# Performance work log

Hardware: AMD Instinct MI355X
Metric: run time of the kernel (lower is better)

Reference implementation:

```python
import jax, jax.numpy as jnp
import numpy as np

# Config constants (mirroring repo globals C.*)
B, L, D = 128, 200, 256          # batch, history length, d_model
NT = 10000                        # num_types (items)
NU = 50000                        # C.USER_NUMBER
NL = 4                            # n_layers
BETA_1 = 0.1                      # C.BETA_1


def _l2norm(x, eps):
    n = jnp.linalg.norm(x, axis=-1, keepdims=True)
    return x / jnp.maximum(n, eps)


def setup_inputs() -> dict:
    key = jax.random.key(0)
    ks = jax.random.split(key, 7)
    user_id = jax.random.randint(ks[0], (B,), 1, NU)
    event_type = jax.random.randint(ks[1], (B, L), 1, NT + 1)  # 1..NT (non-pad)
    adjacent_matrix = jax.random.uniform(ks[2], (NT, NT), jnp.float32)
    pop_encoding = jax.random.normal(ks[3], (NT + 1, D), jnp.float32) * 0.02
    event_emb_w = (jax.random.normal(ks[4], (NT + 1, D), jnp.float32) * 0.02).at[0].set(0.0)
    user_emb_w = (jax.random.normal(ks[5], (NU, D), jnp.float32) * 0.02).at[0].set(0.0)
    layer_ws = jax.random.normal(ks[6], (NL, D, D), jnp.float32) * 0.05
    return {"user_id": user_id, "event_type": event_type,
            "adjacent_matrix": adjacent_matrix, "pop_encoding": pop_encoding,
            "event_emb_w": event_emb_w, "user_emb_w": user_emb_w,
            "layer_ws": layer_ws}


def reference(user_id, event_type, adjacent_matrix, pop_encoding,
              event_emb_w, user_emb_w, layer_ws):
    # non-pad mask (pad idx = 0)
    non_pad = (event_type != 0).astype(jnp.float32)[..., None]  # (B,L,1)

    enc = event_emb_w[event_type]                 # (B,L,D)
    user = user_emb_w[user_id]                    # (B,D)
    pop = pop_encoding[event_type] * non_pad      # (B,L,D)

    # user-specific disentanglement: enc += sign(enc) * normalize(user)
    enc = enc + jnp.sign(enc) * _l2norm(user, 1e-12)[:, None, :]

    # batched adjacency gather: adj[b] = A[e-1][:, e-1] + A[e-1, e-1] (row-broadcast)
    idx = event_type - 1                          # (B,L)
    adj = adjacent_matrix[idx[:, :, None], idx[:, None, :]]      # (B,L,L)
    adj = adj + adjacent_matrix[idx, idx][:, None, :]            # diag broadcast over rows

    # hGCN layer stack: x <- leaky_relu((adj @ x) @ W)
    for i in range(NL):
        enc = jax.nn.leaky_relu(jnp.einsum('bls,bsd->bld', adj, enc) @ layer_ws[i])

    output = enc.mean(axis=1)                     # (B,D)
    user_embeddings = jnp.concatenate([output, pop.mean(axis=1) * BETA_1], axis=-1)  # (B,2D)

    # Predictor (evaluation=True path)
    item_encoding = event_emb_w[1:]               # (NT,D)
    out = user_embeddings[:, :D] @ item_encoding.T  # (B,NT)
    out = _l2norm(out, 1e-5)
    prediction = jnp.tanh(out)
    return prediction, user_embeddings, pop
```

## Files before the change

kernel.cpp:

```cpp
#include <hip/hip_runtime.h>
#include <math.h>

#define B_ 128
#define L_ 200
#define D_ 256
#define NT_ 10000
#define NL_ 4
#define BETA1 0.1f

typedef _Float16 f16x8 __attribute__((ext_vector_type(8)));
typedef _Float16 f16x4 __attribute__((ext_vector_type(4)));
typedef float f32x4 __attribute__((ext_vector_type(4)));

struct HL { _Float16 h, l; };
__device__ __forceinline__ HL split2v(float v) {
    HL r;
    r.h = (_Float16)v;
    r.l = (_Float16)(v - (float)r.h);
    return r;
}

__device__ __forceinline__ float getscale(const unsigned int* amax, int i, int extra) {
    float am = fmaxf(__uint_as_float(amax[i]), 1e-30f);
    return scalbnf(1.f, 6 - ilogbf(am) - extra);
}

__global__ void user_norm_kernel(const int* __restrict__ user_id,
                                 const float* __restrict__ user_emb_w,
                                 float* __restrict__ unorm,
                                 unsigned int* __restrict__ amax) {
    int b = blockIdx.x;
    int d = threadIdx.x;
    if (b == 0 && d < 16) amax[d] = 0u;
    int uid = user_id[b];
    float v = user_emb_w[(long)uid * D_ + d];
    float sq = v * v;
    for (int off = 32; off > 0; off >>= 1) sq += __shfl_down(sq, off, 64);
    __shared__ float s[4];
    int wid = d >> 6, lane = d & 63;
    if (lane == 0) s[wid] = sq;
    __syncthreads();
    float n = sqrtf(s[0] + s[1] + s[2] + s[3]);
    n = fmaxf(n, 1e-12f);
    unorm[b * D_ + d] = v / n;
}

__global__ void enc0pop_kernel(const int* __restrict__ event_type,
                               const float* __restrict__ E,
                               const float* __restrict__ pope,
                               const float* __restrict__ unorm,
                               float* __restrict__ encF,
                               float* __restrict__ pop_out,
                               unsigned int* __restrict__ amax) {
    int d = threadIdx.x;
    float m = 0.f;
    for (int bl = blockIdx.x; bl < B_ * L_; bl += gridDim.x) {
        int b = bl / L_;
        int et = event_type[bl];
        float e = E[(long)et * D_ + d];
        float sg = (e > 0.f) ? 1.f : ((e < 0.f) ? -1.f : 0.f);
        float u = unorm[b * D_ + d];
        float v = e + sg * u;
        encF[(long)bl * D_ + d] = v;
        m = fmaxf(m, fabsf(v));
        pop_out[(long)bl * D_ + d] = (et != 0) ? pope[(long)et * D_ + d] : 0.f;
    }
    for (int off = 32; off > 0; off >>= 1) m = fmaxf(m, __shfl_down(m, off, 64));
    __shared__ float sm[4];
    int wid = d >> 6, lane = d & 63;
    if (lane == 0) sm[wid] = m;
    __syncthreads();
    if (d == 0)
        atomicMax(amax, __float_as_uint(fmaxf(fmaxf(sm[0], sm[1]), fmaxf(sm[2], sm[3]))));
}

__global__ void diag_kernel(const int* __restrict__ event_type,
                            const float* __restrict__ A,
                            float* __restrict__ diag) {
    int i = blockIdx.x * blockDim.x + threadIdx.x;
    if (i >= B_ * L_) return;
    long idx = (long)event_type[i] - 1;
    diag[i] = A[idx * NT_ + idx];
}

__global__ void adj_split_kernel(const int* __restrict__ event_type,
                                 const float* __restrict__ A,
                                 const float* __restrict__ diag,
                                 _Float16* __restrict__ adjH,
                                 _Float16* __restrict__ adjL) {
    int b = blockIdx.y;
    int i0 = blockIdx.x * 4;
    int j = threadIdx.x;
    __shared__ int sidx[L_];
    __shared__ float sdiag[L_];
    if (j < L_) {
        sidx[j]  = event_type[b * L_ + j] - 1;
        sdiag[j] = diag[b * L_ + j];
    }
    __syncthreads();
    if (j >= L_) return;
    float dj = sdiag[j];
    int cj = sidx[j];
#pragma unroll
    for (int r = 0; r < 4; r++) {
        int i = i0 + r;
        float v = A[(long)sidx[i] * NT_ + cj] + dj;
        HL s = split2v(v);
        long o = ((long)b * L_ + i) * L_ + j;
        adjH[o] = s.h; adjL[o] = s.l;
    }
}

__global__ void wsplit_kernel(const float* __restrict__ W,
                              _Float16* __restrict__ WTh,
                              _Float16* __restrict__ WTl) {
    int layer = blockIdx.z;
    int k0 = blockIdx.y * 64, n0 = blockIdx.x * 64;
    const float* Wl = W + (long)layer * D_ * D_;
    __shared__ float t[64][65];
    int tid = threadIdx.x;
    for (int i = 0; i < 16; i++) {
        int idx = i * 256 + tid;
        int k = idx >> 6, n = idx & 63;
        t[k][n] = Wl[(long)(k0 + k) * D_ + n0 + n];
    }
    __syncthreads();
    for (int i = 0; i < 16; i++) {
        int idx = i * 256 + tid;
        int n = idx >> 6, k = idx & 63;
        float v = t[k][n];
        long o = (long)layer * D_ * D_ + (long)(n0 + n) * D_ + (k0 + k);
        HL r = split2v(v);
        WTh[o] = r.h; WTl[o] = r.l;
    }
}

__global__ void esplit_kernel(const float* __restrict__ E,
                              _Float16* __restrict__ ETh,
                              _Float16* __restrict__ ETl) {
    long f = ((long)blockIdx.x * 256 + threadIdx.x) * 4;
    float4 v = *(const float4*)(E + D_ + f);
    f16x4 h, l;
    HL r0 = split2v(v.x); h[0] = r0.h; l[0] = r0.l;
    HL r1 = split2v(v.y); h[1] = r1.h; l[1] = r1.l;
    HL r2 = split2v(v.z); h[2] = r2.h; l[2] = r2.l;
    HL r3 = split2v(v.w); h[3] = r3.h; l[3] = r3.l;
    *(f16x4*)(ETh + f) = h;
    *(f16x4*)(ETl + f) = l;
}

__global__ __launch_bounds__(256) void gemm1_kernel(
    const _Float16* __restrict__ adjH, const _Float16* __restrict__ adjL,
    const float* __restrict__ encF,
    _Float16* __restrict__ tmpH, _Float16* __restrict__ tmpL,
    const unsigned int* __restrict__ amax, int layer) {
    int b = blockIdx.z;
    const _Float16* Ah = adjH + (long)b * L_ * L_;
    const _Float16* Al = adjL + (long)b * L_ * L_;
    const float*    Bf = encF + (long)b * L_ * D_;
    int m0 = blockIdx.y * 128, n0 = blockIdx.x * 128;
    int tid = threadIdx.x, lane = tid & 63, wid = tid >> 6;
    int wr = wid >> 1, wc = wid & 1;
    float scale = getscale(amax, layer, 0);

    __shared__ _Float16 sAh[128][40], sAl[128][40];
    __shared__ _Float16 sBh[128][40], sBl[128][40];

    f32x4 acc[4][4] = {};
    int fr = lane & 15, kb = (lane >> 4) * 8, fq = lane >> 4;

    for (int k0 = 0; k0 < L_; k0 += 32) {
#pragma unroll
        for (int c = 0; c < 2; c++) {
            int idx = c * 256 + tid;
            int row = idx >> 2, kq = (idx & 3) * 8;
            int gk = k0 + kq;
            f16x8 vh = {}, vl = {};
            if (m0 + row < L_ && gk < L_) {
                long o = (long)(m0 + row) * L_ + gk;
                vh = *(const f16x8*)(Ah + o);
                vl = *(const f16x8*)(Al + o);
            }
            *(f16x8*)&sAh[row][kq] = vh;
            *(f16x8*)&sAl[row][kq] = vl;
        }
#pragma unroll
        for (int q2 = 0; q2 < 2; q2++) {
            int item = q2 * 256 + tid;
            int n = item & 127;
            int oct = item >> 7;
            int gk0 = k0 + oct * 8;
            f16x8 h, l;
#pragma unroll
            for (int q = 0; q < 8; q++) {
                int gk = gk0 + q;
                float v = (gk < L_) ? Bf[(long)gk * D_ + n0 + n] * scale : 0.f;
                HL r = split2v(v);
                h[q] = r.h; l[q] = r.l;
            }
            *(f16x8*)&sBh[n][oct * 8] = h;
            *(f16x8*)&sBl[n][oct * 8] = l;
        }
        __syncthreads();

        f16x8 fbh[4], fbl[4];
#pragma unroll
        for (int n = 0; n < 4; n++) {
            int rB = wc * 64 + n * 16 + fr;
            fbh[n] = *(const f16x8*)&sBh[rB][kb];
            fbl[n] = *(const f16x8*)&sBl[rB][kb];
        }
#pragma unroll
        for (int m = 0; m < 4; m++) {
            int rA = wr * 64 + m * 16 + fr;
            f16x8 fah = *(const f16x8*)&sAh[rA][kb];
            f16x8 fal = *(const f16x8*)&sAl[rA][kb];
#pragma unroll
            for (int n = 0; n < 4; n++) {
                acc[m][n] = __builtin_amdgcn_mfma_f32_16x16x32_f16(fah, fbh[n], acc[m][n], 0, 0, 0);
                acc[m][n] = __builtin_amdgcn_mfma_f32_16x16x32_f16(fah, fbl[n], acc[m][n], 0, 0, 0);
                acc[m][n] = __builtin_amdgcn_mfma_f32_16x16x32_f16(fal, fbh[n], acc[m][n], 0, 0, 0);
            }
        }
        __syncthreads();
    }

    _Float16* Ch = tmpH + (long)b * L_ * D_;
    _Float16* Cl = tmpL + (long)b * L_ * D_;
#pragma unroll
    for (int m = 0; m < 4; m++)
#pragma unroll
        for (int n = 0; n < 4; n++)
#pragma unroll
            for (int r = 0; r < 4; r++) {
                int row = m0 + wr * 64 + m * 16 + fq * 4 + r;
                int col = n0 + wc * 64 + n * 16 + fr;
                if (row < L_) {
                    HL s = split2v(acc[m][n][r]);
                    long o = (long)row * D_ + col;
                    Ch[o] = s.h; Cl[o] = s.l;
                }
            }
}

__global__ __launch_bounds__(256) void gemm2_kernel(
    const _Float16* __restrict__ Ah, const _Float16* __restrict__ Al,
    const _Float16* __restrict__ Bh, const _Float16* __restrict__ Bl,
    float* __restrict__ Cf, unsigned int* __restrict__ amax) {
    int m0 = blockIdx.y * 128, n0 = blockIdx.x * 128;
    int tid = threadIdx.x, lane = tid & 63, wid = tid >> 6;
    int wr = wid >> 1, wc = wid & 1;
    __shared__ _Float16 sAh[128][40], sAl[128][40];
    __shared__ _Float16 sBh[128][40], sBl[128][40];
    __shared__ float sRed[4];
    f32x4 acc[4][4] = {};
    int fr = lane & 15, kb = (lane >> 4) * 8, fq = lane >> 4;

    for (int k0 = 0; k0 < D_; k0 += 32) {
#pragma unroll
        for (int c = 0; c < 2; c++) {
            int idx = c * 256 + tid;
            int row = idx >> 2, kq = (idx & 3) * 8, gk = k0 + kq;
            long oa = (long)(m0 + row) * D_ + gk;
            *(f16x8*)&sAh[row][kq] = *(const f16x8*)(Ah + oa);
            *(f16x8*)&sAl[row][kq] = *(const f16x8*)(Al + oa);
            long ob = (long)(n0 + row) * D_ + gk;
            *(f16x8*)&sBh[row][kq] = *(const f16x8*)(Bh + ob);
            *(f16x8*)&sBl[row][kq] = *(const f16x8*)(Bl + ob);
        }
        __syncthreads();
        f16x8 fbh[4], fbl[4];
#pragma unroll
        for (int n = 0; n < 4; n++) {
            int rB = wc * 64 + n * 16 + fr;
            fbh[n] = *(const f16x8*)&sBh[rB][kb];
            fbl[n] = *(const f16x8*)&sBl[rB][kb];
        }
#pragma unroll
        for (int m = 0; m < 4; m++) {
            int rA = wr * 64 + m * 16 + fr;
            f16x8 fah = *(const f16x8*)&sAh[rA][kb];
            f16x8 fal = *(const f16x8*)&sAl[rA][kb];
#pragma unroll
            for (int n = 0; n < 4; n++) {
                acc[m][n] = __builtin_amdgcn_mfma_f32_16x16x32_f16(fah, fbh[n], acc[m][n], 0, 0, 0);
                acc[m][n] = __builtin_amdgcn_mfma_f32_16x16x32_f16(fah, fbl[n], acc[m][n], 0, 0, 0);
                acc[m][n] = __builtin_amdgcn_mfma_f32_16x16x32_f16(fal, fbh[n], acc[m][n], 0, 0, 0);
            }
        }
        __syncthreads();
    }

    float tmax = 0.f;
#pragma unroll
    for (int m = 0; m < 4; m++)
#pragma unroll
        for (int n = 0; n < 4; n++)
#pragma unroll
            for (int r = 0; r < 4; r++) {
                int row = m0 + wr * 64 + m * 16 + fq * 4 + r;
                int col = n0 + wc * 64 + n * 16 + fr;
                float v = acc[m][n][r];
                v = (v >= 0.f) ? v : 0.01f * v;
                Cf[(long)row * D_ + col] = v;
                tmax = fmaxf(tmax, fabsf(v));
            }
    for (int off = 32; off > 0; off >>= 1) tmax = fmaxf(tmax, __shfl_down(tmax, off, 64));
    if (lane == 0) sRed[wid] = tmax;
    __syncthreads();
    if (tid == 0)
        atomicMax(amax, __float_as_uint(fmaxf(fmaxf(sRed[0], sRed[1]), fmaxf(sRed[2], sRed[3]))));
}

__global__ __launch_bounds__(1024) void mean_fused_kernel(
    const float* __restrict__ encF,
    const int* __restrict__ event_type,
    const float* __restrict__ pope,
    const unsigned int* __restrict__ amax,
    float* __restrict__ ue,
    _Float16* __restrict__ ueh,
    _Float16* __restrict__ uel) {
    int b = blockIdx.x, tid = threadIdx.x;
    int c = tid >> 8, d = tid & 255;
    float s1 = 0.f, s2 = 0.f;
    int l0 = c * 50;
    for (int l = l0; l < l0 + 50; l++) {
        s1 += encF[((long)b * L_ + l) * D_ + d];
        int et = event_type[b * L_ + l];
        s2 += (et != 0) ? pope[(long)et * D_ + d] : 0.f;
    }
    __shared__ float red1[4][256], red2[4][256];
    red1[c][d] = s1;
    red2[c][d] = s2;
    __syncthreads();
    if (c == 0) {
        s1 = red1[0][d] + red1[1][d] + red1[2][d] + red1[3][d];
        s2 = red2[0][d] + red2[1][d] + red2[2][d] + red2[3][d];
        float S = 1.f;
        for (int i = 0; i < NL_; i++) S *= getscale(amax, i, 0);
        ue[b * 2 * D_ + d]      = s1 / (float)L_ / S;
        ue[b * 2 * D_ + D_ + d] = s2 * (BETA1 / (float)L_);
        float sc = getscale(amax, NL_, 8);
        HL r = split2v(s1 * sc);
        ueh[b * D_ + d] = r.h;
        uel[b * D_ + d] = r.l;
    }
}

__global__ __launch_bounds__(256) void pred_mfma_kernel(
    const _Float16* __restrict__ Ah, const _Float16* __restrict__ Al,
    const _Float16* __restrict__ Bh, const _Float16* __restrict__ Bl,
    float* __restrict__ Cf) {
    int n0 = blockIdx.x * 64;
    int tid = threadIdx.x, lane = tid & 63, wid = tid >> 6;
    int wr = wid >> 1, wc = wid & 1;
    __shared__ _Float16 sAh[128][40], sAl[128][40];
    __shared__ _Float16 sBh[64][40], sBl[64][40];
    f32x4 acc[4][2] = {};
    int fr = lane & 15, kb = (lane >> 4) * 8, fq = lane >> 4;

    for (int k0 = 0; k0 < D_; k0 += 32) {
#pragma unroll
        for (int c = 0; c < 2; c++) {
            int idx = c * 256 + tid;
            int row = idx >> 2, kq = (idx & 3) * 8, gk = k0 + kq;
            long oa = (long)row * D_ + gk;
            *(f16x8*)&sAh[row][kq] = *(const f16x8*)(Ah + oa);
            *(f16x8*)&sAl[row][kq] = *(const f16x8*)(Al + oa);
        }
        {
            int row = tid >> 2, kq = (tid & 3) * 8, gk = k0 + kq;
            f16x8 wh = {}, wl = {};
            if (n0 + row < NT_) {
                long ob = (long)(n0 + row) * D_ + gk;
                wh = *(const f16x8*)(Bh + ob);
                wl = *(const f16x8*)(Bl + ob);
            }
            *(f16x8*)&sBh[row][kq] = wh;
            *(f16x8*)&sBl[row][kq] = wl;
        }
        __syncthreads();
        f16x8 fbh[2], fbl[2];
#pragma unroll
        for (int n = 0; n < 2; n++) {
            int rB = wc * 32 + n * 16 + fr;
            fbh[n] = *(const f16x8*)&sBh[rB][kb];
            fbl[n] = *(const f16x8*)&sBl[rB][kb];
        }
#pragma unroll
        for (int m = 0; m < 4; m++) {
            int rA = wr * 64 + m * 16 + fr;
            f16x8 fah = *(const f16x8*)&sAh[rA][kb];
            f16x8 fal = *(const f16x8*)&sAl[rA][kb];
#pragma unroll
            for (int n = 0; n < 2; n++) {
                acc[m][n] = __builtin_amdgcn_mfma_f32_16x16x32_f16(fah, fbh[n], acc[m][n], 0, 0, 0);
                acc[m][n] = __builtin_amdgcn_mfma_f32_16x16x32_f16(fah, fbl[n], acc[m][n], 0, 0, 0);
                acc[m][n] = __builtin_amdgcn_mfma_f32_16x16x32_f16(fal, fbh[n], acc[m][n], 0, 0, 0);
            }
        }
        __syncthreads();
    }
#pragma unroll
    for (int m = 0; m < 4; m++)
#pragma unroll
        for (int n = 0; n < 2; n++)
#pragma unroll
            for (int r = 0; r < 4; r++) {
                int row = wr * 64 + m * 16 + fq * 4 + r;
                int col = n0 + wc * 32 + n * 16 + fr;
                if (col < NT_)
                    Cf[(long)row * NT_ + col] = acc[m][n][r];
            }
}

__global__ void normtanh2_kernel(float* __restrict__ pred) {
    int b = blockIdx.x, t = threadIdx.x;
    float* row = pred + (long)b * NT_;
    float v[10];
    float sq = 0.f;
#pragma unroll
    for (int p = 0; p < 10; p++) {
        int i = p * 1024 + t;
        v[p] = (i < NT_) ? row[i] : 0.f;
        sq += v[p] * v[p];
    }
    for (int off = 32; off > 0; off >>= 1) sq += __shfl_down(sq, off, 64);
    __shared__ float s[16];
    if ((t & 63) == 0) s[t >> 6] = sq;
    __syncthreads();
    float n = 0.f;
    for (int i = 0; i < 16; i++) n += s[i];
    float inv = 1.f / fmaxf(sqrtf(n), 1e-5f);
#pragma unroll
    for (int p = 0; p < 10; p++) {
        int i = p * 1024 + t;
        if (i < NT_) row[i] = tanhf(v[p] * inv);
    }
}

__global__ void enc0_kernel(const int* __restrict__ event_type,
                            const float* __restrict__ E,
                            const float* __restrict__ unorm,
                            float* __restrict__ encF) {
    int d = threadIdx.x;
    for (int bl = blockIdx.x; bl < B_ * L_; bl += gridDim.x) {
        int b = bl / L_;
        int et = event_type[bl];
        float e = E[(long)et * D_ + d];
        float sg = (e > 0.f) ? 1.f : ((e < 0.f) ? -1.f : 0.f);
        float u = unorm[b * D_ + d];
        encF[(long)bl * D_ + d] = e + sg * u;
    }
}

__global__ void pop_kernel(const int* __restrict__ event_type,
                           const float* __restrict__ pope,
                           float* __restrict__ pop_out) {
    int bl = blockIdx.x;
    int d = threadIdx.x;
    int et = event_type[bl];
    float np = (et != 0) ? 1.0f : 0.0f;
    pop_out[(long)bl * D_ + d] = pope[(long)et * D_ + d] * np;
}

template <bool BT, bool LEAKY>
__global__ void gemm_kernel(const float* __restrict__ A,
                            const float* __restrict__ Bm,
                            float* __restrict__ C,
                            int M, int N, int K, int lda, int ldb, int ldc,
                            long strideA, long strideB, long strideC) {
    int batch = blockIdx.z;
    A  += (long)batch * strideA;
    Bm += (long)batch * strideB;
    C  += (long)batch * strideC;
    const int BM = 64, BN = 64, BK = 16;
    __shared__ float As[BK][BM + 1];
    __shared__ float Bs[BK][BN + 1];
    int tid = threadIdx.x;
    int m0 = blockIdx.y * BM, n0 = blockIdx.x * BN;
    int tx = tid & 15, ty = tid >> 4;
    float acc[4][4] = {};
    for (int k0 = 0; k0 < K; k0 += BK) {
        {
            int m = tid >> 2, kk = (tid & 3) * 4;
            int gm = m0 + m;
#pragma unroll
            for (int q = 0; q < 4; q++) {
                int gk = k0 + kk + q;
                float x = (gm < M && gk < K) ? A[(long)gm * lda + gk] : 0.f;
                As[kk + q][m] = x;
            }
        }
        if (!BT) {
            int kk = tid >> 4, n = (tid & 15) * 4;
            int gk = k0 + kk;
#pragma unroll
            for (int q = 0; q < 4; q++) {
                int gn = n0 + n + q;
                float x = (gk < K && gn < N) ? Bm[(long)gk * ldb + gn] : 0.f;
                Bs[kk][n + q] = x;
            }
        } else {
            int n = tid >> 2, kk = (tid & 3) * 4;
            int gn = n0 + n;
#pragma unroll
            for (int q = 0; q < 4; q++) {
                int gk = k0 + kk + q;
                float x = (gn < N && gk < K) ? Bm[(long)gn * ldb + gk] : 0.f;
                Bs[kk + q][n] = x;
            }
        }
        __syncthreads();
#pragma unroll
        for (int kk = 0; kk < BK; kk++) {
            float a[4], bv[4];
#pragma unroll
            for (int q = 0; q < 4; q++) a[q] = As[kk][ty * 4 + q];
#pragma unroll
            for (int q = 0; q < 4; q++) bv[q] = Bs[kk][tx * 4 + q];
#pragma unroll
            for (int i = 0; i < 4; i++)
#pragma unroll
                for (int j = 0; j < 4; j++)
                    acc[i][j] += a[i] * bv[j];
        }
        __syncthreads();
    }
#pragma unroll
    for (int i = 0; i < 4; i++) {
        int gm = m0 + ty * 4 + i;
        if (gm >= M) continue;
#pragma unroll
        for (int j = 0; j < 4; j++) {
            int gn = n0 + tx * 4 + j;
            if (gn >= N) continue;
            float v = acc[i][j];
            if (LEAKY) v = (v >= 0.f) ? v : 0.01f * v;
            C[(long)gm * ldc + gn] = v;
        }
    }
}

__global__ void mean_plain_kernel(const float* __restrict__ enc,
                                  const int* __restrict__ event_type,
                                  const float* __restrict__ pope,
                                  float* __restrict__ ue) {
    int b = blockIdx.x, d = threadIdx.x;
    float s1 = 0.f, s2 = 0.f;
    for (int l = 0; l < L_; l++) {
        s1 += enc[((long)b * L_ + l) * D_ + d];
        int et = event_type[b * L_ + l];
        float np = (et != 0) ? 1.0f : 0.0f;
        s2 += pope[(long)et * D_ + d] * np;
    }
    ue[b * (2 * D_) + d]      = s1 / (float)L_;
    ue[b * (2 * D_) + D_ + d] = (s2 / (float)L_) * BETA1;
}

__global__ void adj_kernel_f32(const int* __restrict__ event_type,
                               const float* __restrict__ A,
                               const float* __restrict__ diag,
                               float* __restrict__ adj) {
    int b = blockIdx.y;
    int i = blockIdx.x;
    int j = threadIdx.x;
    __shared__ int sidx[L_];
    __shared__ float sdiag[L_];
    if (j < L_) {
        sidx[j]  = event_type[b * L_ + j] - 1;
        sdiag[j] = diag[b * L_ + j];
    }
    __syncthreads();
    if (j >= L_) return;
    long row = (long)event_type[b * L_ + i] - 1;
    adj[((long)b * L_ + i) * L_ + j] = A[row * NT_ + sidx[j]] + sdiag[j];
}

__global__ void normtanh_kernel(float* __restrict__ pred) {
    int b = blockIdx.x;
    int t = threadIdx.x;
    float* row = pred + (long)b * NT_;
    float sq = 0.f;
    for (int i = t; i < NT_; i += 256) { float v = row[i]; sq += v * v; }
    for (int off = 32; off > 0; off >>= 1) sq += __shfl_down(sq, off, 64);
    __shared__ float s[4];
    int wid = t >> 6, lane = t & 63;
    if (lane == 0) s[wid] = sq;
    __syncthreads();
    float n = sqrtf(s[0] + s[1] + s[2] + s[3]);
    n = fmaxf(n, 1e-5f);
    float inv = 1.f / n;
    for (int i = t; i < NT_; i += 256) row[i] = tanhf(row[i] * inv);
}

extern "C" void kernel_launch(void* const* d_in, const int* in_sizes, int n_in,
                              void* d_out, int out_size, void* d_ws, size_t ws_size,
                              hipStream_t stream) {
    const int*   user_id    = (const int*)d_in[0];
    const int*   event_type = (const int*)d_in[1];
    const float* A          = (const float*)d_in[2];
    const float* pope       = (const float*)d_in[3];
    const float* E          = (const float*)d_in[4];
    const float* U          = (const float*)d_in[5];
    const float* W          = (const float*)d_in[6];

    float* out  = (float*)d_out;
    float* pred = out;
    float* ue   = out + (long)B_ * NT_;
    float* pop  = ue  + (long)B_ * 2 * D_;

    char* w = (char*)d_ws;
    auto carve = [&](size_t bytes) { char* p = w; w += (bytes + 255) & ~(size_t)255; return p; };
    unsigned int* amax = (unsigned int*)carve(64);
    _Float16* adjH  = (_Float16*)carve((size_t)B_ * L_ * L_ * 2);
    _Float16* adjL  = (_Float16*)carve((size_t)B_ * L_ * L_ * 2);
    _Float16* tmpH  = (_Float16*)carve((size_t)B_ * L_ * D_ * 2);
    _Float16* tmpL  = (_Float16*)carve((size_t)B_ * L_ * D_ * 2);
    float*    encF  = (float*)carve((size_t)B_ * L_ * D_ * 4);
    _Float16* WTh   = (_Float16*)carve((size_t)NL_ * D_ * D_ * 2);
    _Float16* WTl   = (_Float16*)carve((size_t)NL_ * D_ * D_ * 2);
    _Float16* ETh   = (_Float16*)carve((size_t)NT_ * D_ * 2);
    _Float16* ETl   = (_Float16*)carve((size_t)NT_ * D_ * 2);
    _Float16* ueh   = (_Float16*)carve((size_t)B_ * D_ * 2);
    _Float16* uel   = (_Float16*)carve((size_t)B_ * D_ * 2);
    float*    unorm = (float*)carve((size_t)B_ * D_ * 4);
    float*    diag  = (float*)carve((size_t)B_ * L_ * 4);
    size_t needed = (size_t)(w - (char*)d_ws);

    if (ws_size >= needed) {
        user_norm_kernel<<<B_, 256, 0, stream>>>(user_id, U, unorm, amax);
        enc0pop_kernel<<<1280, 256, 0, stream>>>(event_type, E, pope, unorm, encF, pop, amax);
        diag_kernel<<<(B_ * L_ + 255) / 256, 256, 0, stream>>>(event_type, A, diag);
        adj_split_kernel<<<dim3(50, B_), 256, 0, stream>>>(event_type, A, diag, adjH, adjL);
        wsplit_kernel<<<dim3(4, 4, NL_), 256, 0, stream>>>(W, WTh, WTl);
        esplit_kernel<<<NT_ * D_ / 1024, 256, 0, stream>>>(E, ETh, ETl);

        for (int i = 0; i < NL_; i++) {
            gemm1_kernel<<<dim3(2, 2, B_), 256, 0, stream>>>(
                adjH, adjL, encF, tmpH, tmpL, amax, i);
            gemm2_kernel<<<dim3(2, B_ * L_ / 128), 256, 0, stream>>>(
                tmpH, tmpL, WTh + (long)i * D_ * D_, WTl + (long)i * D_ * D_,
                encF, amax + i + 1);
        }

        mean_fused_kernel<<<B_, 1024, 0, stream>>>(encF, event_type, pope, amax, ue, ueh, uel);
        pred_mfma_kernel<<<(NT_ + 63) / 64, 256, 0, stream>>>(ueh, uel, ETh, ETl, pred);
        normtanh2_kernel<<<B_, 1024, 0, stream>>>(pred);
    } else {
        float* ws0   = (float*)d_ws;
        float* uno   = ws0;
        float* dia   = uno + B_ * D_;
        float* adjF  = dia + B_ * L_;
        float* encA2 = adjF + (long)B_ * L_ * L_;
        float* encB2 = encA2 + (long)B_ * L_ * D_;
        float* tmp   = pop;

        user_norm_kernel<<<B_, 256, 0, stream>>>(user_id, U, uno, (unsigned int*)dia);
        enc0_kernel<<<1280, 256, 0, stream>>>(event_type, E, uno, encA2);
        diag_kernel<<<(B_ * L_ + 255) / 256, 256, 0, stream>>>(event_type, A, dia);
        adj_kernel_f32<<<dim3(L_, B_), 256, 0, stream>>>(event_type, A, dia, adjF);

        float* cur = encA2; float* nxt = encB2;
        for (int i = 0; i < NL_; i++) {
            dim3 g1((D_ + 63) / 64, (L_ + 63) / 64, B_);
            gemm_kernel<false, false><<<g1, 256, 0, stream>>>(
                adjF, cur, tmp, L_, D_, L_, L_, D_, D_,
                (long)L_ * L_, (long)L_ * D_, (long)L_ * D_);
            dim3 g2((D_ + 63) / 64, (B_ * L_ + 63) / 64, 1);
            gemm_kernel<false, true><<<g2, 256, 0, stream>>>(
                tmp, W + (long)i * D_ * D_, nxt, B_ * L_, D_, D_, D_, D_, D_, 0, 0, 0);
            float* t = cur; cur = nxt; nxt = t;
        }
        pop_kernel<<<B_ * L_, 256, 0, stream>>>(event_type, pope, pop);
        mean_plain_kernel<<<B_, 256, 0, stream>>>(cur, event_type, pope, ue);

        dim3 g3((NT_ + 63) / 64, (B_ + 63) / 64, 1);
        gemm_kernel<true, false><<<g3, 256, 0, stream>>>(
            ue, E + D_, pred, B_, NT_, D_, 2 * D_, D_, NT_, 0, 0, 0);
        normtanh_kernel<<<B_, 256, 0, stream>>>(pred);
    }
}
```

Before: 394.2 us.

## Halve gemm1 N-tile and register-prefetch next K-slice during MFMA

The batched adj@enc GEMM now uses a 128x64 output tile instead of 128x128, doubling the grid from 512 to 1024 blocks for better CU occupancy. The main loop also prefetches the next K-slice of A (fp16 hi/lo) and B (fp32) into registers before the MFMA work, overlapping global loads with compute. The cost is more register pressure, and A tiles are reloaded twice as often across blocks.

```diff
diff --git a/kernel.cpp b/kernel.cpp
--- a/kernel.cpp
+++ b/kernel.cpp
@@ -158,55 +158,79 @@
     const _Float16* Ah = adjH + (long)b * L_ * L_;
     const _Float16* Al = adjL + (long)b * L_ * L_;
     const float*    Bf = encF + (long)b * L_ * D_;
-    int m0 = blockIdx.y * 128, n0 = blockIdx.x * 128;
+    int m0 = blockIdx.y * 128, n0 = blockIdx.x * 64;
     int tid = threadIdx.x, lane = tid & 63, wid = tid >> 6;
     int wr = wid >> 1, wc = wid & 1;
     float scale = getscale(amax, layer, 0);
 
     __shared__ _Float16 sAh[128][40], sAl[128][40];
-    __shared__ _Float16 sBh[128][40], sBl[128][40];
-
-    f32x4 acc[4][4] = {};
+    __shared__ _Float16 sBh[64][40], sBl[64][40];
+
+    f32x4 acc[4][2] = {};
     int fr = lane & 15, kb = (lane >> 4) * 8, fq = lane >> 4;
-
-    for (int k0 = 0; k0 < L_; k0 += 32) {
+    int nB = tid & 63, octB = tid >> 6;
+
+    f16x8 pAh[2], pAl[2];
+    float pB[8];
+#pragma unroll
+    for (int c = 0; c < 2; c++) {
+        int idx = c * 256 + tid;
+        int row = idx >> 2, kq = (idx & 3) * 8;
+        f16x8 vh = {}, vl = {};
+        if (m0 + row < L_ && kq < L_) {
+            long o = (long)(m0 + row) * L_ + kq;
+            vh = *(const f16x8*)(Ah + o);
+            vl = *(const f16x8*)(Al + o);
+        }
+        pAh[c] = vh; pAl[c] = vl;
+    }
+#pragma unroll
+    for (int q = 0; q < 8; q++) {
+        int gk = octB * 8 + q;
+        pB[q] = (gk < L_) ? Bf[(long)gk * D_ + n0 + nB] * scale : 0.f;
+    }
+
+    for (int it = 0; it < 7; it++) {
 #pragma unroll
         for (int c = 0; c < 2; c++) {
             int idx = c * 256 + tid;
             int row = idx >> 2, kq = (idx & 3) * 8;
-            int gk = k0 + kq;
-            f16x8 vh = {}, vl = {};
-            if (m0 + row < L_ && gk < L_) {
-                long o = (long)(m0 + row) * L_ + gk;
-                vh = *(const f16x8*)(Ah + o);
-                vl = *(const f16x8*)(Al + o);
-            }
-            *(f16x8*)&sAh[row][kq] = vh;
-            *(f16x8*)&sAl[row][kq] = vl;
-        }
-#pragma unroll
-        for (int q2 = 0; q2 < 2; q2++) {
-            int item = q2 * 256 + tid;
-            int n = item & 127;
-            int oct = item >> 7;
-            int gk0 = k0 + oct * 8;
+            *(f16x8*)&sAh[row][kq] = pAh[c];
+            *(f16x8*)&sAl[row][kq] = pAl[c];
+        }
+        {
             f16x8 h, l;
 #pragma unroll
+            for (int q = 0; q < 8; q++) { HL r = split2v(pB[q]); h[q] = r.h; l[q] = r.l; }
+            *(f16x8*)&sBh[nB][octB * 8] = h;
+            *(f16x8*)&sBl[nB][octB * 8] = l;
+        }
+        __syncthreads();
+        if (it < 6) {
+            int k1 = (it + 1) * 32;
+#pragma unroll
+            for (int c = 0; c < 2; c++) {
+                int idx = c * 256 + tid;
+                int row = idx >> 2, kq = (idx & 3) * 8;
+                int gk = k1 + kq;
+                f16x8 vh = {}, vl = {};
+                if (m0 + row < L_ && gk < L_) {
+                    long o = (long)(m0 + row) * L_ + gk;
+                    vh = *(const f16x8*)(Ah + o);
+                    vl = *(const f16x8*)(Al + o);
+                }
+                pAh[c] = vh; pAl[c] = vl;
+            }
+#pragma unroll
             for (int q = 0; q < 8; q++) {
-                int gk = gk0 + q;
-                float v = (gk < L_) ? Bf[(long)gk * D_ + n0 + n] * scale : 0.f;
-                HL r = split2v(v);
-                h[q] = r.h; l[q] = r.l;
-            }
-            *(f16x8*)&sBh[n][oct * 8] = h;
-            *(f16x8*)&sBl[n][oct * 8] = l;
-        }
-        __syncthreads();
-
-        f16x8 fbh[4], fbl[4];
-#pragma unroll
-        for (int n = 0; n < 4; n++) {
-            int rB = wc * 64 + n * 16 + fr;
+                int gk = k1 + octB * 8 + q;
+                pB[q] = (gk < L_) ? Bf[(long)gk * D_ + n0 + nB] * scale : 0.f;
+            }
+        }
+        f16x8 fbh[2], fbl[2];
+#pragma unroll
+        for (int n = 0; n < 2; n++) {
+            int rB = wc * 32 + n * 16 + fr;
             fbh[n] = *(const f16x8*)&sBh[rB][kb];
             fbl[n] = *(const f16x8*)&sBl[rB][kb];
         }
@@ -216,7 +240,7 @@
             f16x8 fah = *(const f16x8*)&sAh[rA][kb];
             f16x8 fal = *(const f16x8*)&sAl[rA][kb];
 #pragma unroll
-            for (int n = 0; n < 4; n++) {
+            for (int n = 0; n < 2; n++) {
                 acc[m][n] = __builtin_amdgcn_mfma_f32_16x16x32_f16(fah, fbh[n], acc[m][n], 0, 0, 0);
                 acc[m][n] = __builtin_amdgcn_mfma_f32_16x16x32_f16(fah, fbl[n], acc[m][n], 0, 0, 0);
                 acc[m][n] = __builtin_amdgcn_mfma_f32_16x16x32_f16(fal, fbh[n], acc[m][n], 0, 0, 0);
@@ -230,11 +254,11 @@
 #pragma unroll
     for (int m = 0; m < 4; m++)
 #pragma unroll
-        for (int n = 0; n < 4; n++)
+        for (int n = 0; n < 2; n++)
 #pragma unroll
             for (int r = 0; r < 4; r++) {
                 int row = m0 + wr * 64 + m * 16 + fq * 4 + r;
-                int col = n0 + wc * 64 + n * 16 + fr;
+                int col = n0 + wc * 32 + n * 16 + fr;
                 if (row < L_) {
                     HL s = split2v(acc[m][n][r]);
                     long o = (long)row * D_ + col;
@@ -637,7 +661,7 @@
         esplit_kernel<<<NT_ * D_ / 1024, 256, 0, stream>>>(E, ETh, ETl);
 
         for (int i = 0; i < NL_; i++) {
-            gemm1_kernel<<<dim3(2, 2, B_), 256, 0, stream>>>(
+            gemm1_kernel<<<dim3(4, 2, B_), 256, 0, stream>>>(
                 adjH, adjL, encF, tmpH, tmpL, amax, i);
             gemm2_kernel<<<dim3(2, B_ * L_ / 128), 256, 0, stream>>>(
                 tmpH, tmpL, WTh + (long)i * D_ * D_, WTl + (long)i * D_ * D_,
```

After: 493.6 us. 25.2% more time.
